# Optimization experiments

Hardware: AMD Instinct MI355X
Metric: run time of the kernel (lower is better)

## Reference

```python
import jax, jax.numpy as jnp
import numpy as np

TAU_MEM, TAU_SYN = 20.0, 5.0
THRESHOLD, BETA, RESET = 1.0, 4.0, 0.0
ALPHA_MEM = float(np.exp(-1.0 / TAU_MEM))
ALPHA_SYN = float(np.exp(-1.0 / TAU_SYN))
EPS = 1e-6


def _lif(x, W, b):
    # x: [B,T,D] -> spikes_with_grad: [B,T,H] (faithful to original incl. the
    # spikes + stop_grad(spikes - surrogate) expression, forward value 2*s - sg)
    cur = jnp.einsum('btd,dh->bth', x, W) + b  # all-timestep projection (same math as per-step dense)
    B, T, H = cur.shape
    v0 = jnp.zeros((B, H), cur.dtype)
    i0 = jnp.zeros((B, H), cur.dtype)

    def step(carry, ic):
        v, i = carry
        i = ALPHA_SYN * i + ic
        v = ALPHA_MEM * v + (1.0 - ALPHA_MEM) * i
        spikes = (v >= THRESHOLD).astype(jnp.float32)
        sg = BETA / (2.0 * (1.0 + jnp.cosh(BETA * (v - THRESHOLD))))
        swg = spikes + jax.lax.stop_gradient(spikes - sg)
        v = jnp.where(spikes > 0, RESET, v)
        return (v, i), swg

    (_, _), out = jax.lax.scan(step, (v0, i0), cur.transpose(1, 0, 2))
    return out.transpose(1, 0, 2)


def _layernorm(x, scale, bias):
    mu = jnp.mean(x, axis=-1, keepdims=True)
    var = jnp.var(x, axis=-1, keepdims=True)
    return (x - mu) * jax.lax.rsqrt(var + EPS) * scale + bias


def setup_inputs() -> dict:
    key = jax.random.key(0)
    ks = jax.random.split(key, 8)
    B, T, D = 512, 128, 512
    H0, H1, H2, C = 256, 128, 64, 2
    s = 0.02
    return {
        'spike_trains': jax.random.uniform(ks[0], (B, T, D), jnp.float32),
        'W0': jax.random.normal(ks[1], (D, H0), jnp.float32) * s,
        'b0': jnp.zeros((H0,), jnp.float32),
        'ln1_scale': jnp.ones((H0,), jnp.float32),
        'ln1_bias': jnp.zeros((H0,), jnp.float32),
        'W1': jax.random.normal(ks[2], (H0, H1), jnp.float32) * s,
        'b1': jnp.zeros((H1,), jnp.float32),
        'ln2_scale': jnp.ones((H1,), jnp.float32),
        'ln2_bias': jnp.zeros((H1,), jnp.float32),
        'W2': jax.random.normal(ks[3], (H1, H2), jnp.float32) * s,
        'b2': jnp.zeros((H2,), jnp.float32),
        'Wc': jax.random.normal(ks[4], (H2, C), jnp.float32) * s,
        'bc': jnp.zeros((C,), jnp.float32),
    }


def reference(spike_trains, W0, b0, ln1_scale, ln1_bias, W1, b1,
              ln2_scale, ln2_bias, W2, b2, Wc, bc):
    x = _lif(spike_trains, W0, b0)                    # layer 0: no pre-norm
    x = _lif(_layernorm(x, ln1_scale, ln1_bias), W1, b1)
    x = _lif(_layernorm(x, ln2_scale, ln2_bias), W2, b2)
    pooled = jnp.mean(x, axis=1)                      # [B, H2]
    logits = pooled @ Wc + bc                         # [B, C]
    return logits, pooled, jnp.mean(x)
```

## Files before the change

### kernel.cpp

```cpp
#include <hip/hip_runtime.h>
#include <cstddef>

static constexpr float A_MEM  = 0.951229424500714f;
static constexpr float A_SYN  = 0.8187307530779818f;
static constexpr float OM_MEM = 0.04877057549928599f;

template<int BM, int BN, int K, bool LN>
__global__ __launch_bounds__(256, 1) void gemm_ln(
    const float* __restrict__ A, const float* __restrict__ W,
    const float* __restrict__ bias,
    const float2* __restrict__ stats, const float* __restrict__ lnsc,
    const float* __restrict__ lnbi, float* __restrict__ C)
{
  constexpr int BK   = 16;
  constexpr int S    = K / BK;
  constexpr int PA   = BM + 4;
  constexpr int NTYG = BM / 8;
  constexpr int NTX  = 256 / NTYG;
  constexpr int CJ4  = BN / (NTX * 4);
  constexpr int APT  = BM / 64;
  constexpr int WPT  = BN / 64;

  __shared__ float As[BK][PA];
  __shared__ float Ws[BK][BN];

  const int tid = threadIdx.x;
  const int tx  = tid % NTX;
  const int ty  = tid / NTX;
  const int m0  = blockIdx.x * BM;

  float4 aR[APT], wR[WPT];

  auto load_tile = [&](int k0) {
    #pragma unroll
    for (int p = 0; p < APT; ++p) {
      int idx = tid + p * 256;
      int r = idx >> 2, c4 = (idx & 3) << 2;
      float4 a = *(const float4*)(A + (size_t)(m0 + r) * K + k0 + c4);
      if constexpr (LN) {
        float2 st = stats[m0 + r];
        float4 ls = *(const float4*)(lnsc + k0 + c4);
        float4 lb = *(const float4*)(lnbi + k0 + c4);
        a.x = (a.x - st.x) * st.y * ls.x + lb.x;
        a.y = (a.y - st.x) * st.y * ls.y + lb.y;
        a.z = (a.z - st.x) * st.y * ls.z + lb.z;
        a.w = (a.w - st.x) * st.y * ls.w + lb.w;
      }
      aR[p] = a;
    }
    #pragma unroll
    for (int p = 0; p < WPT; ++p) {
      int idx = tid + p * 256;
      int k = idx / (BN / 4), c4 = (idx % (BN / 4)) << 2;
      wR[p] = *(const float4*)(W + (size_t)(k0 + k) * BN + c4);
    }
  };

  auto store_tile = [&]() {
    #pragma unroll
    for (int p = 0; p < APT; ++p) {
      int idx = tid + p * 256;
      int r = idx >> 2, c4 = (idx & 3) << 2;
      As[c4 + 0][r] = aR[p].x;
      As[c4 + 1][r] = aR[p].y;
      As[c4 + 2][r] = aR[p].z;
      As[c4 + 3][r] = aR[p].w;
    }
    #pragma unroll
    for (int p = 0; p < WPT; ++p) {
      int idx = tid + p * 256;
      int k = idx / (BN / 4), c4 = (idx % (BN / 4)) << 2;
      *(float4*)&Ws[k][c4] = wR[p];
    }
  };

  float acc[8][CJ4 * 4];
  #pragma unroll
  for (int i = 0; i < 8; ++i)
    #pragma unroll
    for (int j = 0; j < CJ4 * 4; ++j) acc[i][j] = 0.f;

  load_tile(0);
  for (int s = 0; s < S; ++s) {
    __syncthreads();
    store_tile();
    __syncthreads();
    if (s + 1 < S) load_tile((s + 1) * BK);
    asm volatile("" ::: "memory");
    #pragma unroll
    for (int kk = 0; kk < BK; ++kk) {
      float4 a0 = *(const float4*)&As[kk][ty * 8];
      float4 a1 = *(const float4*)&As[kk][ty * 8 + 4];
      float av[8] = {a0.x, a0.y, a0.z, a0.w, a1.x, a1.y, a1.z, a1.w};
      float4 wv[CJ4];
      #pragma unroll
      for (int j = 0; j < CJ4; ++j)
        wv[j] = *(const float4*)&Ws[kk][tx * 4 + j * NTX * 4];
      #pragma unroll
      for (int i = 0; i < 8; ++i)
        #pragma unroll
        for (int j = 0; j < CJ4; ++j) {
          acc[i][4 * j + 0] += av[i] * wv[j].x;
          acc[i][4 * j + 1] += av[i] * wv[j].y;
          acc[i][4 * j + 2] += av[i] * wv[j].z;
          acc[i][4 * j + 3] += av[i] * wv[j].w;
        }
    }
  }

  #pragma unroll
  for (int j = 0; j < CJ4; ++j) {
    int col = tx * 4 + j * NTX * 4;
    float4 bb = *(const float4*)(bias + col);
    #pragma unroll
    for (int i = 0; i < 8; ++i) {
      int row = m0 + ty * 8 + i;
      float4 o;
      o.x = acc[i][4 * j + 0] + bb.x;
      o.y = acc[i][4 * j + 1] + bb.y;
      o.z = acc[i][4 * j + 2] + bb.z;
      o.w = acc[i][4 * j + 3] + bb.w;
      *(float4*)(C + (size_t)row * BN + col) = o;
    }
  }
}

template<int H, int BPB>
__global__ __launch_bounds__(256) void lif_stats(
    float* __restrict__ cur, float2* __restrict__ stats)
{
  constexpr int T = 128;
  constexpr int WPB = H / 64;
  const int tid  = threadIdx.x;
  const int h    = tid % H;
  const size_t b = (size_t)blockIdx.x * BPB + tid / H;
  float* p = cur + b * T * H + h;
  __shared__ float w1[4][T], w2[4][T];
  const int wv = tid >> 6, lane = tid & 63;
  float v = 0.f, ci = 0.f;
  for (int t0 = 0; t0 < T; t0 += 4) {
    float ic[4];
    #pragma unroll
    for (int u = 0; u < 4; ++u) ic[u] = p[(size_t)(t0 + u) * H];
    #pragma unroll
    for (int u = 0; u < 4; ++u) {
      ci = A_SYN * ci + ic[u];
      v  = A_MEM * v + OM_MEM * ci;
      bool sp = v >= 1.0f;
      float xx = 4.0f * (v - 1.0f);
      float e  = __expf(xx);
      float tp = 1.0f + e;
      float sg = 4.0f * e / (tp * tp);
      float o  = (sp ? 2.0f : 0.0f) - sg;
      v = sp ? 0.0f : v;
      ic[u] = o;
      float s1 = o, s2 = o * o;
      #pragma unroll
      for (int off = 1; off < 64; off <<= 1) {
        s1 += __shfl_xor(s1, off);
        s2 += __shfl_xor(s2, off);
      }
      if (lane == 0) { w1[wv][t0 + u] = s1; w2[wv][t0 + u] = s2; }
    }
    #pragma unroll
    for (int u = 0; u < 4; ++u) p[(size_t)(t0 + u) * H] = ic[u];
  }
  __syncthreads();
  if (tid < T * BPB) {
    int t  = tid & (T - 1);
    int bs = tid >> 7;
    float s1 = 0.f, s2 = 0.f;
    #pragma unroll
    for (int w = 0; w < WPB; ++w) {
      s1 += w1[bs * WPB + w][t];
      s2 += w2[bs * WPB + w][t];
    }
    float mu  = s1 * (1.0f / H);
    float var = s2 * (1.0f / H) - mu * mu;
    float rs  = rsqrtf(var + 1e-6f);
    stats[((size_t)blockIdx.x * BPB + bs) * T + t] = make_float2(mu, rs);
  }
}

__global__ __launch_bounds__(256) void lif_pool(
    const float* __restrict__ cur, float* __restrict__ pooled)
{
  constexpr int T = 128, H = 64;
  int flat = blockIdx.x * 256 + threadIdx.x;
  int b = flat >> 6, h = flat & 63;
  const float* p = cur + (size_t)b * T * H + h;
  float v = 0.f, ci = 0.f, sum = 0.f;
  for (int t0 = 0; t0 < T; t0 += 4) {
    float ic[4];
    #pragma unroll
    for (int u = 0; u < 4; ++u) ic[u] = p[(size_t)(t0 + u) * H];
    #pragma unroll
    for (int u = 0; u < 4; ++u) {
      ci = A_SYN * ci + ic[u];
      v  = A_MEM * v + OM_MEM * ci;
      bool sp = v >= 1.0f;
      float xx = 4.0f * (v - 1.0f);
      float e  = __expf(xx);
      float tp = 1.0f + e;
      float sg = 4.0f * e / (tp * tp);
      sum += (sp ? 2.0f : 0.0f) - sg;
      v = sp ? 0.0f : v;
    }
  }
  pooled[flat] = sum * (1.0f / 128.0f);
}

__global__ __launch_bounds__(1024) void head_k(
    const float* __restrict__ pooled, const float* __restrict__ Wc,
    const float* __restrict__ bc, float* __restrict__ logits,
    float* __restrict__ meanp)
{
  const int tid = threadIdx.x;
  const int b = tid >> 1, c = tid & 1;
  float accl = 0.f;
  #pragma unroll 8
  for (int k = 0; k < 64; ++k) accl += pooled[b * 64 + k] * Wc[k * 2 + c];
  logits[tid] = accl + bc[c];

  float s = 0.f;
  for (int i2 = tid; i2 < 512 * 64; i2 += 1024) s += pooled[i2];
  #pragma unroll
  for (int off = 32; off; off >>= 1) s += __shfl_xor(s, off);
  __shared__ float red[16];
  const int wave = tid >> 6, lane = tid & 63;
  if (lane == 0) red[wave] = s;
  __syncthreads();
  if (tid == 0) {
    float tot = 0.f;
    #pragma unroll
    for (int w = 0; w < 16; ++w) tot += red[w];
    meanp[0] = tot * (1.0f / 32768.0f);
  }
}

extern "C" void kernel_launch(void* const* d_in, const int* in_sizes, int n_in,
                              void* d_out, int out_size, void* d_ws, size_t ws_size,
                              hipStream_t stream) {
  const float* x    = (const float*)d_in[0];
  const float* W0   = (const float*)d_in[1];
  const float* b0   = (const float*)d_in[2];
  const float* ln1s = (const float*)d_in[3];
  const float* ln1b = (const float*)d_in[4];
  const float* W1   = (const float*)d_in[5];
  const float* b1   = (const float*)d_in[6];
  const float* ln2s = (const float*)d_in[7];
  const float* ln2b = (const float*)d_in[8];
  const float* W2   = (const float*)d_in[9];
  const float* b2   = (const float*)d_in[10];
  const float* Wc   = (const float*)d_in[11];
  const float* bc   = (const float*)d_in[12];

  float* out    = (float*)d_out;
  float* logits = out;
  float* pooled = out + 1024;
  float* meanp  = out + 1024 + 32768;

  char* ws = (char*)d_ws;
  float*  cur0   = (float*)ws;
  float*  cur1   = (float*)(ws + (size_t)64 * 1024 * 1024);
  float*  cur2   = (float*)(ws + (size_t)96 * 1024 * 1024);
  float2* stats0 = (float2*)(ws + (size_t)112 * 1024 * 1024);
  float2* stats1 = (float2*)(ws + (size_t)112 * 1024 * 1024 + 524288);

  gemm_ln<64, 256, 512, false><<<1024, 256, 0, stream>>>(
      x, W0, b0, nullptr, nullptr, nullptr, cur0);
  lif_stats<256, 1><<<512, 256, 0, stream>>>(cur0, stats0);
  gemm_ln<64, 128, 256, true><<<1024, 256, 0, stream>>>(
      cur0, W1, b1, stats0, ln1s, ln1b, cur1);
  lif_stats<128, 2><<<256, 256, 0, stream>>>(cur1, stats1);
  gemm_ln<128, 64, 128, true><<<512, 256, 0, stream>>>(
      cur1, W2, b2, stats1, ln2s, ln2b, cur2);
  lif_pool<<<128, 256, 0, stream>>>(cur2, pooled);
  head_k<<<1, 1024, 0, stream>>>(pooled, Wc, bc, logits, meanp);
}
```

Before: 688.6 us.

## Retile GEMMs to 128-row blocks with 2D grid and 8x8 thread tiles

Replaces the GEMM kernel with a 128-row tile whose grid also splits N, so the first layer uses two 128-column blocks instead of one 256-wide block. Each thread now owns a contiguous 8x8 (or 8x4) output tile and reads it from shared memory as float4. Occupancy hint rises to 2 blocks per SM. The aim is more A reuse per block, fewer registers per thread, and better latency hiding. The trade-off is that layer 0 now reads each A row twice across the two column blocks.

```diff
diff --git a/kernel.cpp b/kernel.cpp
--- a/kernel.cpp
+++ b/kernel.cpp
@@ -5,122 +5,130 @@
 static constexpr float A_SYN  = 0.8187307530779818f;
 static constexpr float OM_MEM = 0.04877057549928599f;
 
-template<int BM, int BN, int K, bool LN>
-__global__ __launch_bounds__(256, 1) void gemm_ln(
+__device__ inline float4 ln4(float4 a, float2 st, float4 ls, float4 lb) {
+  a.x = (a.x - st.x) * st.y * ls.x + lb.x;
+  a.y = (a.y - st.x) * st.y * ls.y + lb.y;
+  a.z = (a.z - st.x) * st.y * ls.z + lb.z;
+  a.w = (a.w - st.x) * st.y * ls.w + lb.w;
+  return a;
+}
+
+template<int BN, int K, int N, bool LN>
+__global__ __launch_bounds__(256, 2) void gemm8(
     const float* __restrict__ A, const float* __restrict__ W,
-    const float* __restrict__ bias,
-    const float2* __restrict__ stats, const float* __restrict__ lnsc,
-    const float* __restrict__ lnbi, float* __restrict__ C)
-{
-  constexpr int BK   = 16;
-  constexpr int S    = K / BK;
-  constexpr int PA   = BM + 4;
-  constexpr int NTYG = BM / 8;
-  constexpr int NTX  = 256 / NTYG;
-  constexpr int CJ4  = BN / (NTX * 4);
-  constexpr int APT  = BM / 64;
-  constexpr int WPT  = BN / 64;
+    const float* __restrict__ bias, const float2* __restrict__ stats,
+    const float* __restrict__ lnsc, const float* __restrict__ lnbi,
+    float* __restrict__ C)
+{
+  constexpr int BM = 128, BK = 16;
+  constexpr int PA = BM + 4;
+  constexpr int NJ = BN / 16;
+  constexpr int S  = K / BK;
+  constexpr int WPT = (BK * BN) / 1024;
 
   __shared__ float As[BK][PA];
   __shared__ float Ws[BK][BN];
 
   const int tid = threadIdx.x;
-  const int tx  = tid % NTX;
-  const int ty  = tid / NTX;
-  const int m0  = blockIdx.x * BM;
-
-  float4 aR[APT], wR[WPT];
-
-  auto load_tile = [&](int k0) {
-    #pragma unroll
-    for (int p = 0; p < APT; ++p) {
-      int idx = tid + p * 256;
-      int r = idx >> 2, c4 = (idx & 3) << 2;
-      float4 a = *(const float4*)(A + (size_t)(m0 + r) * K + k0 + c4);
-      if constexpr (LN) {
-        float2 st = stats[m0 + r];
-        float4 ls = *(const float4*)(lnsc + k0 + c4);
-        float4 lb = *(const float4*)(lnbi + k0 + c4);
-        a.x = (a.x - st.x) * st.y * ls.x + lb.x;
-        a.y = (a.y - st.x) * st.y * ls.y + lb.y;
-        a.z = (a.z - st.x) * st.y * ls.z + lb.z;
-        a.w = (a.w - st.x) * st.y * ls.w + lb.w;
-      }
-      aR[p] = a;
-    }
-    #pragma unroll
-    for (int p = 0; p < WPT; ++p) {
-      int idx = tid + p * 256;
-      int k = idx / (BN / 4), c4 = (idx % (BN / 4)) << 2;
-      wR[p] = *(const float4*)(W + (size_t)(k0 + k) * BN + c4);
-    }
-  };
-
-  auto store_tile = [&]() {
-    #pragma unroll
-    for (int p = 0; p < APT; ++p) {
-      int idx = tid + p * 256;
-      int r = idx >> 2, c4 = (idx & 3) << 2;
-      As[c4 + 0][r] = aR[p].x;
-      As[c4 + 1][r] = aR[p].y;
-      As[c4 + 2][r] = aR[p].z;
-      As[c4 + 3][r] = aR[p].w;
-    }
-    #pragma unroll
-    for (int p = 0; p < WPT; ++p) {
-      int idx = tid + p * 256;
-      int k = idx / (BN / 4), c4 = (idx % (BN / 4)) << 2;
-      *(float4*)&Ws[k][c4] = wR[p];
-    }
-  };
-
-  float acc[8][CJ4 * 4];
+  const int tx  = tid & 15;
+  const int ty  = tid >> 4;
+  const int m0  = blockIdx.y * BM;
+  const int n0  = blockIdx.x * BN;
+
+  const int ar0 = tid >> 2;
+  const int ar1 = ar0 + 64;
+  const int ac4 = (tid & 3) << 2;
+  const float* Ap0 = A + (size_t)(m0 + ar0) * K + ac4;
+  const float* Ap1 = A + (size_t)(m0 + ar1) * K + ac4;
+  float2 st0, st1;
+  if constexpr (LN) { st0 = stats[m0 + ar0]; st1 = stats[m0 + ar1]; }
+
+  const int wr0 = tid / (BN / 4);
+  const int wc0 = (tid % (BN / 4)) << 2;
+  constexpr int WRS = 1024 / BN;
+
+  float4 aP0, aP1, wP0, wP1;
+
+  aP0 = *(const float4*)(Ap0);
+  aP1 = *(const float4*)(Ap1);
+  if constexpr (LN) {
+    float4 ls = *(const float4*)(lnsc + ac4);
+    float4 lb = *(const float4*)(lnbi + ac4);
+    aP0 = ln4(aP0, st0, ls, lb);
+    aP1 = ln4(aP1, st1, ls, lb);
+  }
+  wP0 = *(const float4*)(W + (size_t)wr0 * N + n0 + wc0);
+  if constexpr (WPT == 2)
+    wP1 = *(const float4*)(W + (size_t)(wr0 + WRS) * N + n0 + wc0);
+
+  float acc[8][NJ];
   #pragma unroll
   for (int i = 0; i < 8; ++i)
     #pragma unroll
-    for (int j = 0; j < CJ4 * 4; ++j) acc[i][j] = 0.f;
-
-  load_tile(0);
+    for (int j = 0; j < NJ; ++j) acc[i][j] = 0.f;
+
   for (int s = 0; s < S; ++s) {
     __syncthreads();
-    store_tile();
+    As[ac4 + 0][ar0] = aP0.x;
+    As[ac4 + 1][ar0] = aP0.y;
+    As[ac4 + 2][ar0] = aP0.z;
+    As[ac4 + 3][ar0] = aP0.w;
+    As[ac4 + 0][ar1] = aP1.x;
+    As[ac4 + 1][ar1] = aP1.y;
+    As[ac4 + 2][ar1] = aP1.z;
+    As[ac4 + 3][ar1] = aP1.w;
+    *(float4*)&Ws[wr0][wc0] = wP0;
+    if constexpr (WPT == 2) *(float4*)&Ws[wr0 + WRS][wc0] = wP1;
     __syncthreads();
-    if (s + 1 < S) load_tile((s + 1) * BK);
-    asm volatile("" ::: "memory");
+
+    if (s + 1 < S) {
+      const int k0 = (s + 1) * BK;
+      aP0 = *(const float4*)(Ap0 + k0);
+      aP1 = *(const float4*)(Ap1 + k0);
+      if constexpr (LN) {
+        float4 ls = *(const float4*)(lnsc + k0 + ac4);
+        float4 lb = *(const float4*)(lnbi + k0 + ac4);
+        aP0 = ln4(aP0, st0, ls, lb);
+        aP1 = ln4(aP1, st1, ls, lb);
+      }
+      wP0 = *(const float4*)(W + (size_t)(k0 + wr0) * N + n0 + wc0);
+      if constexpr (WPT == 2)
+        wP1 = *(const float4*)(W + (size_t)(k0 + wr0 + WRS) * N + n0 + wc0);
+    }
+
     #pragma unroll
     for (int kk = 0; kk < BK; ++kk) {
       float4 a0 = *(const float4*)&As[kk][ty * 8];
       float4 a1 = *(const float4*)&As[kk][ty * 8 + 4];
       float av[8] = {a0.x, a0.y, a0.z, a0.w, a1.x, a1.y, a1.z, a1.w};
-      float4 wv[CJ4];
-      #pragma unroll
-      for (int j = 0; j < CJ4; ++j)
-        wv[j] = *(const float4*)&Ws[kk][tx * 4 + j * NTX * 4];
+      float wv[NJ];
+      float4 w0 = *(const float4*)&Ws[kk][tx * NJ];
+      wv[0] = w0.x; wv[1] = w0.y; wv[2] = w0.z; wv[3] = w0.w;
+      if constexpr (NJ == 8) {
+        float4 w1 = *(const float4*)&Ws[kk][tx * NJ + 4];
+        wv[4] = w1.x; wv[5] = w1.y; wv[6] = w1.z; wv[7] = w1.w;
+      }
       #pragma unroll
       for (int i = 0; i < 8; ++i)
         #pragma unroll
-        for (int j = 0; j < CJ4; ++j) {
-          acc[i][4 * j + 0] += av[i] * wv[j].x;
-          acc[i][4 * j + 1] += av[i] * wv[j].y;
-          acc[i][4 * j + 2] += av[i] * wv[j].z;
-          acc[i][4 * j + 3] += av[i] * wv[j].w;
-        }
+        for (int j = 0; j < NJ; ++j)
+          acc[i][j] += av[i] * wv[j];
     }
   }
 
   #pragma unroll
-  for (int j = 0; j < CJ4; ++j) {
-    int col = tx * 4 + j * NTX * 4;
+  for (int j4 = 0; j4 < NJ / 4; ++j4) {
+    int col = n0 + tx * NJ + j4 * 4;
     float4 bb = *(const float4*)(bias + col);
     #pragma unroll
     for (int i = 0; i < 8; ++i) {
       int row = m0 + ty * 8 + i;
       float4 o;
-      o.x = acc[i][4 * j + 0] + bb.x;
-      o.y = acc[i][4 * j + 1] + bb.y;
-      o.z = acc[i][4 * j + 2] + bb.z;
-      o.w = acc[i][4 * j + 3] + bb.w;
-      *(float4*)(C + (size_t)row * BN + col) = o;
+      o.x = acc[i][j4 * 4 + 0] + bb.x;
+      o.y = acc[i][j4 * 4 + 1] + bb.y;
+      o.z = acc[i][j4 * 4 + 2] + bb.z;
+      o.w = acc[i][j4 * 4 + 3] + bb.w;
+      *(float4*)(C + (size_t)row * N + col) = o;
     }
   }
 }
@@ -262,18 +270,18 @@
 
   char* ws = (char*)d_ws;
   float*  cur0   = (float*)ws;
-  float*  cur1   = (float*)(ws + (size_t)64 * 1024 * 1024);
-  float*  cur2   = (float*)(ws + (size_t)96 * 1024 * 1024);
-  float2* stats0 = (float2*)(ws + (size_t)112 * 1024 * 1024);
-  float2* stats1 = (float2*)(ws + (size_t)112 * 1024 * 1024 + 524288);
-
-  gemm_ln<64, 256, 512, false><<<1024, 256, 0, stream>>>(
+  float*  cur1   = (float*)(ws + ((size_t)64 << 20));
+  float*  cur2   = (float*)(ws + ((size_t)96 << 20));
+  float2* stats0 = (float2*)(ws + ((size_t)112 << 20));
+  float2* stats1 = (float2*)(ws + ((size_t)112 << 20) + (512 << 10));
+
+  gemm8<128, 512, 256, false><<<dim3(2, 512), 256, 0, stream>>>(
       x, W0, b0, nullptr, nullptr, nullptr, cur0);
   lif_stats<256, 1><<<512, 256, 0, stream>>>(cur0, stats0);
-  gemm_ln<64, 128, 256, true><<<1024, 256, 0, stream>>>(
+  gemm8<128, 256, 128, true><<<dim3(1, 512), 256, 0, stream>>>(
       cur0, W1, b1, stats0, ln1s, ln1b, cur1);
   lif_stats<128, 2><<<256, 256, 0, stream>>>(cur1, stats1);
-  gemm_ln<128, 64, 128, true><<<512, 256, 0, stream>>>(
+  gemm8<64, 128, 64, true><<<dim3(1, 512), 256, 0, stream>>>(
       cur1, W2, b2, stats1, ln2s, ln2b, cur2);
   lif_pool<<<128, 256, 0, stream>>>(cur2, pooled);
   head_k<<<1, 1024, 0, stream>>>(pooled, Wc, bc, logits, meanp);
```

Result: faster. 572.3 us (-16.9%).
